# Kernel tuning notes

Measured on AMD Instinct MI355X. Metric: run time of the kernel, lower is better.

The kernel has to match this reference:

```python
import jax, jax.numpy as jnp
import numpy as np

B, NP, K = 8, 512, 64   # graphs, points per graph, knn neighbors
N = B * NP              # total nodes
EPS = 1e-5


def knn_edges(pos):
    """knn_graph(pos, k=K, batch, loop=True): edges (src=j neighbor, dst=i)."""
    p = pos.reshape(B, NP, 3)
    d2 = jnp.sum((p[:, :, None, :] - p[:, None, :, :]) ** 2, axis=-1)  # [B,NP,NP]
    _, idx = jax.lax.top_k(-d2, K)  # [B,NP,K] nearest (self included, d2=0)
    off = (jnp.arange(B, dtype=jnp.int32) * NP)[:, None, None]
    src = (idx.astype(jnp.int32) + off).reshape(-1)
    dst = jnp.broadcast_to(jnp.arange(NP, dtype=jnp.int32)[None, :, None] + off,
                           (B, NP, K)).reshape(-1)
    return src, dst


def graph_norm(x, batch, w, b, ms):
    """PyG GraphNorm: per-graph mean/std with learnable mean scale."""
    cnt = jax.ops.segment_sum(jnp.ones((x.shape[0], 1), x.dtype), batch, B)
    mean = jax.ops.segment_sum(x, batch, B) / cnt
    out = x - mean[batch] * ms
    var = jax.ops.segment_sum(out * out, batch, B) / cnt
    return w * out / jnp.sqrt(var + EPS)[batch] + b


def pointnet_layer(h, pos, src, dst, w1, b1, w2, b2):
    """message = MLP(concat(h_j, pos_j - pos_i)); aggregate = scatter-max over dst."""
    m = jnp.concatenate([h[src], pos[src] - pos[dst]], axis=-1)  # [E, Cin+3]
    m = jax.nn.relu(m @ w1 + b1) @ w2 + b2                        # [E, Cout]
    return jax.ops.segment_max(m, dst, N)


def _forward(batch, pos,
             gn1_w, gn1_b, gn1_ms, gn2_w, gn2_b, gn2_ms, gn3_w, gn3_b, gn3_ms,
             gn4_w, gn4_b, gn4_ms, gn5_w, gn5_b, gn5_ms, gn6_w, gn6_b, gn6_ms,
             c1_w1, c1_b1, c1_w2, c1_b2, c2_w1, c2_b1, c2_w2, c2_b2,
             c3_w1, c3_b1, c3_w2, c3_b2, c4_w1, c4_b1, c4_w2, c4_b2,
             c5_w1, c5_b1, c5_w2, c5_b2, cls_w, cls_b):
    src, dst = knn_edges(pos)
    h = graph_norm(pos, batch, gn1_w, gn1_b, gn1_ms)
    h = pointnet_layer(h, pos, src, dst, c1_w1, c1_b1, c1_w2, c1_b2)
    h = jax.nn.relu(graph_norm(h, batch, gn2_w, gn2_b, gn2_ms))
    h = pointnet_layer(h, pos, src, dst, c2_w1, c2_b1, c2_w2, c2_b2)
    h = jax.nn.relu(graph_norm(h, batch, gn3_w, gn3_b, gn3_ms))
    h = pointnet_layer(h, pos, src, dst, c3_w1, c3_b1, c3_w2, c3_b2)
    h = jax.nn.relu(graph_norm(h, batch, gn4_w, gn4_b, gn4_ms))
    h = pointnet_layer(h, pos, src, dst, c4_w1, c4_b1, c4_w2, c4_b2)
    h = jax.nn.relu(graph_norm(h, batch, gn5_w, gn5_b, gn5_ms))
    h = pointnet_layer(h, pos, src, dst, c5_w1, c5_b1, c5_w2, c5_b2)
    h = jax.nn.relu(graph_norm(h, batch, gn6_w, gn6_b, gn6_ms))
    return h @ cls_w + cls_b  # [N, 14]


def setup_inputs() -> dict:
    key = jax.random.key(0)
    ks = iter(jax.random.split(key, 40))
    inp = {}
    inp["pos"] = jax.random.normal(next(ks), (N, 3), jnp.float32)
    inp["batch"] = jnp.repeat(jnp.arange(B, dtype=jnp.int32), NP)
    for i, c in enumerate([3, 64, 128, 256, 512, 512], 1):
        inp[f"gn{i}_w"] = jnp.ones((c,), jnp.float32)
        inp[f"gn{i}_b"] = jnp.zeros((c,), jnp.float32)
        inp[f"gn{i}_ms"] = jnp.ones((c,), jnp.float32)
    for i, (ci, co) in enumerate([(3, 64), (64, 128), (128, 256), (256, 512), (512, 512)], 1):
        fin = ci + 3
        inp[f"c{i}_w1"] = jax.random.normal(next(ks), (fin, co), jnp.float32) / np.sqrt(fin).astype(np.float32)
        inp[f"c{i}_b1"] = jnp.zeros((co,), jnp.float32)
        inp[f"c{i}_w2"] = jax.random.normal(next(ks), (co, co), jnp.float32) / np.sqrt(co).astype(np.float32)
        inp[f"c{i}_b2"] = jnp.zeros((co,), jnp.float32)
    inp["cls_w"] = jax.random.normal(next(ks), (512, 14), jnp.float32) / np.float32(np.sqrt(512))
    inp["cls_b"] = jnp.zeros((14,), jnp.float32)
    return inp


def reference(pos, batch,
              gn1_w, gn1_b, gn1_ms, gn2_w, gn2_b, gn2_ms, gn3_w, gn3_b, gn3_ms,
              gn4_w, gn4_b, gn4_ms, gn5_w, gn5_b, gn5_ms, gn6_w, gn6_b, gn6_ms,
              c1_w1, c1_b1, c1_w2, c1_b2, c2_w1, c2_b1, c2_w2, c2_b2,
              c3_w1, c3_b1, c3_w2, c3_b2, c4_w1, c4_b1, c4_w2, c4_b2,
              c5_w1, c5_b1, c5_w2, c5_b2, cls_w, cls_b):
    return _forward(batch, pos,
                    gn1_w, gn1_b, gn1_ms, gn2_w, gn2_b, gn2_ms, gn3_w, gn3_b, gn3_ms,
                    gn4_w, gn4_b, gn4_ms, gn5_w, gn5_b, gn5_ms, gn6_w, gn6_b, gn6_ms,
                    c1_w1, c1_b1, c1_w2, c1_b2, c2_w1, c2_b1, c2_w2, c2_b2,
                    c3_w1, c3_b1, c3_w2, c3_b2, c4_w1, c4_b1, c4_w2, c4_b2,
                    c5_w1, c5_b1, c5_w2, c5_b2, cls_w, cls_b)
```

## Files before the change

### kernel.cpp

```cpp
#include <hip/hip_runtime.h>
#include <stdint.h>

#define N_NODES 4096
#define NGRAPH 8
#define NPTS 512
#define KNN 64
#define EPSN 1e-5f

typedef _Float16 f16x8 __attribute__((ext_vector_type(8)));
typedef float f32x4 __attribute__((ext_vector_type(4)));
typedef unsigned long long u64;

__device__ __forceinline__ unsigned short f2h(float f) {
    _Float16 h = (_Float16)f;
    union { _Float16 h; unsigned short u; } cv; cv.h = h;
    return cv.u;
}

__device__ __forceinline__ void w2cv(const float* __restrict__ src, unsigned short* __restrict__ dst,
                                     int off, int lg2c) {
    int C = 1 << lg2c;
    int k = off >> lg2c, n = off & (C - 1);
    int d = ((n >> 4) * (C / 32) + (k >> 5)) * 512 + ((k >> 3) & 3) * 128 + (n & 15) * 8 + (k & 7);
    dst[d] = f2h(src[off]);
}

__global__ __launch_bounds__(64) void setup_kernel(const float* __restrict__ pos, int* __restrict__ knn_out,
                                                   const float* __restrict__ wa, const float* __restrict__ wb,
                                                   const float* __restrict__ wc, const float* __restrict__ wd,
                                                   const float* __restrict__ we,
                                                   unsigned short* __restrict__ oa, unsigned short* __restrict__ ob,
                                                   unsigned short* __restrict__ oc, unsigned short* __restrict__ od,
                                                   unsigned short* __restrict__ oe,
                                                   float* __restrict__ statz,
                                                   const float* __restrict__ ms1, const float* __restrict__ gw1,
                                                   float* __restrict__ Aa, float* __restrict__ Sa) {
#pragma clang fp contract(off)
    __shared__ float px[NPTS], py[NPTS], pz[NPTS];
    __shared__ u64 keys[NPTS];
    int bid = blockIdx.x;
    int tid = threadIdx.x;
    int gidx = bid * 64 + tid;
    for (int idx = gidx; idx < 40960; idx += 262144) statz[idx] = 0.f;
    for (int idx = gidx; idx < 610304; idx += 262144) {
        if (idx < 4096)        w2cv(wa, oa, idx, 6);
        else if (idx < 20480)  w2cv(wb, ob, idx - 4096, 7);
        else if (idx < 86016)  w2cv(wc, oc, idx - 20480, 8);
        else if (idx < 348160) w2cv(wd, od, idx - 86016, 9);
        else                   w2cv(we, oe, idx - 348160, 9);
    }
    if (bid < 24) {
        int g = bid / 3, ch = bid - g * 3;
        float s1 = 0.f, s2 = 0.f;
        for (int n = tid; n < NPTS; n += 64) {
            float v = pos[(g * NPTS + n) * 3 + ch];
            s1 += v; s2 += v * v;
        }
        #pragma unroll
        for (int off = 32; off; off >>= 1) { s1 += __shfl_xor(s1, off); s2 += __shfl_xor(s2, off); }
        if (tid == 0) {
            float mean = s1 * (1.f / NPTS);
            float av = mean * ms1[ch];
            float var = s2 * (1.f / NPTS) - 2.f * av * mean + av * av;
            Aa[g * 3 + ch] = av;
            Sa[g * 3 + ch] = gw1[ch] / sqrtf(var + EPSN);
        }
    }
    int b = bid >> 9;
    int il = bid & (NPTS - 1);
    for (int n = tid; n < NPTS; n += 64) {
        int base = (b * NPTS + n) * 3;
        px[n] = pos[base]; py[n] = pos[base + 1]; pz[n] = pos[base + 2];
    }
    __syncthreads();
    float xi = px[il], yi = py[il], zi = pz[il];
    for (int n = tid; n < NPTS; n += 64) {
        float dx = px[n] - xi, dy = py[n] - yi, dz = pz[n] - zi;
        float d2 = dx * dx;
        d2 = d2 + dy * dy;
        d2 = d2 + dz * dz;
        keys[n] = (((u64)__float_as_uint(d2)) << 32) | (unsigned)n;
    }
    __syncthreads();
    for (int k2 = 2; k2 <= NPTS; k2 <<= 1) {
        for (int j = k2 >> 1; j > 0; j >>= 1) {
            #pragma unroll 4
            for (int p = 0; p < 4; ++p) {
                int pid = tid + p * 64;
                int t = ((pid & ~(j - 1)) << 1) | (pid & (j - 1));
                int ixj = t | j;
                u64 a = keys[t], c = keys[ixj];
                bool up = ((t & k2) == 0);
                if ((a > c) == up) { keys[t] = c; keys[ixj] = a; }
            }
            __syncthreads();
        }
    }
    int j0 = (int)(keys[tid] & 0xffffffffu);
    knn_out[(size_t)(b * NPTS + il) * KNN + tid] = b * NPTS + j0;
}

template<int CIN, int C, int RELU, int RAW>
__global__ __launch_bounds__(C) void node_kernel(const float* __restrict__ y, const float* __restrict__ pos,
                                                 const float* __restrict__ p1, const float* __restrict__ p2,
                                                 const float* __restrict__ ms, const float* __restrict__ gw,
                                                 const float* __restrict__ bnp,
                                                 const float* __restrict__ w1, const float* __restrict__ b1,
                                                 float* __restrict__ U, float* __restrict__ P) {
    constexpr int ROWS = 16;
    constexpr int KC = 64;
    constexpr int LDH = KC + 4;
    __shared__ float hs[ROWS][LDH];
    __shared__ float As_[CIN > 0 ? CIN : 1], Ss_[CIN > 0 ? CIN : 1];
    const int c = threadIdx.x;
    const int n0 = blockIdx.x * ROWS;
    const int b = n0 >> 9;
    if (RAW) {
        for (int ch = c; ch < CIN; ch += C) {
            float s1 = p1[b * CIN + ch], s2 = p2[b * CIN + ch];
            float mean = s1 * (1.f / NPTS);
            float a = mean * ms[ch];
            float var = s2 * (1.f / NPTS) - 2.f * a * mean + a * a;
            As_[ch] = a;
            Ss_[ch] = gw[ch] / sqrtf(var + EPSN);
        }
    }
    float acc[ROWS];
    #pragma unroll
    for (int r = 0; r < ROWS; ++r) acc[r] = 0.f;
    constexpr int NCHUNK = (CIN + KC - 1) / KC;
    #pragma unroll 1
    for (int s = 0; s < NCHUNK; ++s) {
        const int k0 = s * KC;
        const int kc = (CIN - k0 < KC) ? (CIN - k0) : KC;
        __syncthreads();
        for (int idx = c; idx < ROWS * kc; idx += C) {
            int r = idx / kc, k = idx - r * kc;
            int ch = k0 + k;
            float a = RAW ? As_[ch] : p1[b * CIN + ch];
            float sf = RAW ? Ss_[ch] : p2[b * CIN + ch];
            float v = (y[(size_t)(n0 + r) * CIN + ch] - a) * sf + bnp[ch];
            if (RELU) v = fmaxf(v, 0.f);
            hs[r][k] = v;
        }
        __syncthreads();
        int k = 0;
        for (; k + 4 <= kc; k += 4) {
            float w0 = w1[(size_t)(k0 + k) * C + c];
            float w1v = w1[(size_t)(k0 + k + 1) * C + c];
            float w2v = w1[(size_t)(k0 + k + 2) * C + c];
            float w3v = w1[(size_t)(k0 + k + 3) * C + c];
            #pragma unroll
            for (int r = 0; r < ROWS; ++r) {
                f32x4 hv = *(const f32x4*)&hs[r][k];
                acc[r] = fmaf(hv[0], w0, acc[r]);
                acc[r] = fmaf(hv[1], w1v, acc[r]);
                acc[r] = fmaf(hv[2], w2v, acc[r]);
                acc[r] = fmaf(hv[3], w3v, acc[r]);
            }
        }
        for (; k < kc; ++k) {
            float wv = w1[(size_t)(k0 + k) * C + c];
            #pragma unroll
            for (int r = 0; r < ROWS; ++r)
                acc[r] = fmaf(hs[r][k], wv, acc[r]);
        }
    }
    float pacc[ROWS];
    #pragma unroll
    for (int r = 0; r < ROWS; ++r) pacc[r] = 0.f;
    #pragma unroll
    for (int e = 0; e < 3; ++e) {
        float wv = w1[(size_t)(CIN + e) * C + c];
        #pragma unroll
        for (int r = 0; r < ROWS; ++r)
            pacc[r] = fmaf(pos[(n0 + r) * 3 + e], wv, pacc[r]);
    }
    float bv = b1[c];
    #pragma unroll
    for (int r = 0; r < ROWS; ++r) {
        U[(size_t)(n0 + r) * C + c] = acc[r] + pacc[r] + bv;
        P[(size_t)(n0 + r) * C + c] = pacc[r];
    }
}

template<int C, int W>
__global__ __launch_bounds__(W * 64, 4) void edge_kernel(const float* __restrict__ U, const float* __restrict__ P,
                                                         const int* __restrict__ knn, const unsigned short* __restrict__ w2t,
                                                         const float* __restrict__ b2, float* __restrict__ Y,
                                                         float* __restrict__ sum1, float* __restrict__ sum2) {
    constexpr int NCT = C / (W * 16);
    constexpr int S32 = C / 32;
    constexpr int NCHUNK = C / 8;
    __shared__ unsigned short Th[64 * C];
    __shared__ int jn[64];
    __shared__ float Pr[C];
    const int bid = blockIdx.x;
    const int i = ((bid & 7) << 9) | (bid >> 3);
    const int tid = threadIdx.x;
    const int wave = tid >> 6, lane = tid & 63, m = lane & 15, quad = lane >> 4;
    const int cw = wave * (NCT * 16);
    if (tid < 64) jn[tid] = knn[(size_t)i * KNN + tid];
    for (int idx = tid; idx < C; idx += W * 64) Pr[idx] = P[(size_t)i * C + idx];
    __syncthreads();
    #pragma unroll 2
    for (int idx = tid; idx < 64 * NCHUNK; idx += W * 64) {
        int row = idx / NCHUNK, ch = idx - row * NCHUNK;
        const float* up = U + (size_t)jn[row] * C + ch * 8;
        f32x4 va = *(const f32x4*)up;
        f32x4 vb = *(const f32x4*)(up + 4);
        f32x4 pa = *(const f32x4*)&Pr[ch * 8];
        f32x4 pb = *(const f32x4*)&Pr[ch * 8 + 4];
        uint4 pk;
        pk.x = (unsigned)f2h(fmaxf(va[0] - pa[0], 0.f)) | ((unsigned)f2h(fmaxf(va[1] - pa[1], 0.f)) << 16);
        pk.y = (unsigned)f2h(fmaxf(va[2] - pa[2], 0.f)) | ((unsigned)f2h(fmaxf(va[3] - pa[3], 0.f)) << 16);
        pk.z = (unsigned)f2h(fmaxf(vb[0] - pb[0], 0.f)) | ((unsigned)f2h(fmaxf(vb[1] - pb[1], 0.f)) << 16);
        pk.w = (unsigned)f2h(fmaxf(vb[2] - pb[2], 0.f)) | ((unsigned)f2h(fmaxf(vb[3] - pb[3], 0.f)) << 16);
        int sc = (ch & ~7) | ((ch ^ row) & 7);
        *(uint4*)&Th[row * C + sc * 8] = pk;
    }
    __syncthreads();
    f32x4 acc[4][NCT];
    f32x4 zero = {0.f, 0.f, 0.f, 0.f};
    #pragma unroll
    for (int rt = 0; rt < 4; ++rt)
        #pragma unroll
        for (int ct = 0; ct < NCT; ++ct)
            acc[rt][ct] = zero;
    #pragma unroll 2
    for (int s = 0; s < S32; ++s) {
        f16x8 a[4];
        #pragma unroll
        for (int rt = 0; rt < 4; ++rt) {
            int row = rt * 16 + m;
            int chunk = s * 4 + quad;
            int sc = (chunk & ~7) | ((chunk ^ row) & 7);
            a[rt] = *(const f16x8*)&Th[row * C + sc * 8];
        }
        #pragma unroll
        for (int ct = 0; ct < NCT; ++ct) {
            const f16x8 bb = *(const f16x8*)(w2t +
                (size_t)(((cw >> 4) + ct) * S32 + s) * 512 + quad * 128 + m * 8);
            #pragma unroll
            for (int rt = 0; rt < 4; ++rt)
                acc[rt][ct] = __builtin_amdgcn_mfma_f32_16x16x32_f16(a[rt], bb, acc[rt][ct], 0, 0, 0);
        }
    }
    const int gb = i >> 9;
    #pragma unroll
    for (int ct = 0; ct < NCT; ++ct) {
        float vmax = -3.4e38f;
        #pragma unroll
        for (int rt = 0; rt < 4; ++rt) {
            vmax = fmaxf(vmax, acc[rt][ct][0]);
            vmax = fmaxf(vmax, acc[rt][ct][1]);
            vmax = fmaxf(vmax, acc[rt][ct][2]);
            vmax = fmaxf(vmax, acc[rt][ct][3]);
        }
        vmax = fmaxf(vmax, __shfl_xor(vmax, 16));
        vmax = fmaxf(vmax, __shfl_xor(vmax, 32));
        if (quad == 0) {
            int col = cw + ct * 16 + m;
            float val = vmax + b2[col];
            Y[(size_t)i * C + col] = val;
            atomicAdd(&sum1[gb * C + col], val);
            atomicAdd(&sum2[gb * C + col], val * val);
        }
    }
}

__device__ __forceinline__ uint4 pack8(f32x4 va, f32x4 vb, f32x4 pa, f32x4 pb) {
    uint4 pk;
    pk.x = (unsigned)f2h(fmaxf(va[0] - pa[0], 0.f)) | ((unsigned)f2h(fmaxf(va[1] - pa[1], 0.f)) << 16);
    pk.y = (unsigned)f2h(fmaxf(va[2] - pa[2], 0.f)) | ((unsigned)f2h(fmaxf(va[3] - pa[3], 0.f)) << 16);
    pk.z = (unsigned)f2h(fmaxf(vb[0] - pb[0], 0.f)) | ((unsigned)f2h(fmaxf(vb[1] - pb[1], 0.f)) << 16);
    pk.w = (unsigned)f2h(fmaxf(vb[2] - pb[2], 0.f)) | ((unsigned)f2h(fmaxf(vb[3] - pb[3], 0.f)) << 16);
    return pk;
}

template<int C>
__global__ __launch_bounds__(512, 2) void edgeb_kernel(const float* __restrict__ U, const float* __restrict__ P,
                                                       const int* __restrict__ knn, const unsigned short* __restrict__ w2t,
                                                       const float* __restrict__ b2, float* __restrict__ Y,
                                                       float* __restrict__ sum1, float* __restrict__ sum2) {
    constexpr int NCT = C / 128;
    constexpr int S32 = C / 32;
    constexpr int NCHK = C / 8;
    constexpr int RSTEP = 512 / NCHK;
    __shared__ unsigned short Th[(C / 64) * 128 * 64];
    __shared__ int jn[128];
    const int bid = blockIdx.x;
    const int g = bid & 7;
    const int n0 = (g << 9) | ((bid >> 3) << 1);
    const int tid = threadIdx.x;
    const int lane = tid & 63, wave = tid >> 6, m = lane & 15, quad = lane >> 4;
    const int cw = wave * (NCT * 16);
    if (tid < 128) jn[tid] = knn[(size_t)(n0 + (tid >> 6)) * KNN + (tid & 63)];
    const int ch = tid & (NCHK - 1);
    const int rb = tid / NCHK;
    const int cblk = ch >> 3, cw8 = ch & 7;
    const float* pp = P + (size_t)n0 * C + ch * 8;
    f32x4 pa0 = *(const f32x4*)pp;
    f32x4 pb0 = *(const f32x4*)(pp + 4);
    f32x4 pa1 = *(const f32x4*)(pp + C);
    f32x4 pb1 = *(const f32x4*)(pp + C + 4);
    __syncthreads();
    #pragma unroll 4
    for (int t = 0; t < 128 / RSTEP; ++t) {
        int row = rb + t * RSTEP;
        const float* up = U + (size_t)jn[row] * C + ch * 8;
        f32x4 va = *(const f32x4*)up;
        f32x4 vb = *(const f32x4*)(up + 4);
        f32x4 pa = (row & 64) ? pa1 : pa0;
        f32x4 pb = (row & 64) ? pb1 : pb0;
        *(uint4*)&Th[cblk * 8192 + row * 64 + ((cw8 ^ (row & 7)) << 3)] = pack8(va, vb, pa, pb);
    }
    __syncthreads();
    f32x4 acc[8][NCT];
    f32x4 zero = {0.f, 0.f, 0.f, 0.f};
    #pragma unroll
    for (int rt = 0; rt < 8; ++rt)
        #pragma unroll
        for (int ct = 0; ct < NCT; ++ct)
            acc[rt][ct] = zero;
    const unsigned short* wt = w2t + (size_t)(cw >> 4) * S32 * 512 + quad * 128 + m * 8;
    int idx0[8], idx1[8];
    #pragma unroll
    for (int rt = 0; rt < 8; ++rt) {
        int row = rt * 16 + m;
        idx0[rt] = row * 64 + ((quad ^ (row & 7)) << 3);
        idx1[rt] = row * 64 + (((4 + quad) ^ (row & 7)) << 3);
    }
    const unsigned short* pB[NCT];
    #pragma unroll
    for (int ct = 0; ct < NCT; ++ct)
        pB[ct] = wt + ((size_t)ct * S32 + 2) * 512;
    f16x8 bbA[NCT], bbB[NCT];
    #pragma unroll
    for (int ct = 0; ct < NCT; ++ct) {
        bbA[ct] = *(const f16x8*)(wt + (size_t)ct * S32 * 512);
        bbB[ct] = *(const f16x8*)(wt + ((size_t)ct * S32 + 1) * 512);
    }
    const unsigned short* tcur = Th;
    auto step = [&](f16x8 (&buf)[NCT], const int (&idx)[8], int poff, bool pre) {
        f16x8 a[8];
        #pragma unroll
        for (int rt = 0; rt < 8; ++rt)
            a[rt] = *(const f16x8*)&tcur[idx[rt]];
        #pragma unroll
        for (int ct = 0; ct < NCT; ++ct) {
            f16x8 bcur = buf[ct];
            if (pre) buf[ct] = *(const f16x8*)(pB[ct] + poff);
            __builtin_amdgcn_s_setprio(1);
            #pragma unroll
            for (int rt = 0; rt < 8; ++rt)
                acc[rt][ct] = __builtin_amdgcn_mfma_f32_16x16x32_f16(a[rt], bcur, acc[rt][ct], 0, 0, 0);
            __builtin_amdgcn_s_setprio(0);
        }
    };
    #pragma unroll 1
    for (int s = 0; s + 2 < S32; s += 2) {
        step(bbA, idx0, 0, true);
        step(bbB, idx1, 512, true);
        tcur += 8192;
        #pragma unroll
        for (int ct = 0; ct < NCT; ++ct) pB[ct] += 1024;
    }
    step(bbA, idx0, 0, false);
    step(bbB, idx1, 0, false);
    #pragma unroll
    for (int h = 0; h < 2; ++h) {
        #pragma unroll
        for (int ct = 0; ct < NCT; ++ct) {
            float vmax = -3.4e38f;
            #pragma unroll
            for (int rt = h * 4; rt < h * 4 + 4; ++rt) {
                vmax = fmaxf(vmax, acc[rt][ct][0]);
                vmax = fmaxf(vmax, acc[rt][ct][1]);
                vmax = fmaxf(vmax, acc[rt][ct][2]);
                vmax = fmaxf(vmax, acc[rt][ct][3]);
            }
            vmax = fmaxf(vmax, __shfl_xor(vmax, 16));
            vmax = fmaxf(vmax, __shfl_xor(vmax, 32));
            if (quad == 0) {
                int col = cw + ct * 16 + m;
                float val = vmax + b2[col];
                Y[(size_t)(n0 + h) * C + col] = val;
                atomicAdd(&sum1[g * C + col], val);
                atomicAdd(&sum2[g * C + col], val * val);
            }
        }
    }
}

__global__ __launch_bounds__(256) void cls_kernel(const float* __restrict__ y, const float* __restrict__ sum1,
                                                  const float* __restrict__ sum2, const float* __restrict__ ms,
                                                  const float* __restrict__ gw, const float* __restrict__ gnb,
                                                  const float* __restrict__ w, const float* __restrict__ bias,
                                                  float* __restrict__ out) {
    __shared__ float wl[512 * 14];
    __shared__ _Float16 hn[16][520];
    __shared__ float As[512], Ss[512];
    int tid = threadIdx.x;
    int n0 = blockIdx.x * 16;
    int b = n0 >> 9;
    for (int ch = tid; ch < 512; ch += 256) {
        float s1 = sum1[b * 512 + ch], s2 = sum2[b * 512 + ch];
        float mean = s1 * (1.f / NPTS);
        float a = mean * ms[ch];
        float var = s2 * (1.f / NPTS) - 2.f * a * mean + a * a;
        As[ch] = a;
        Ss[ch] = gw[ch] / sqrtf(var + EPSN);
    }
    for (int idx = tid; idx < 512 * 14; idx += 256) wl[idx] = w[idx];
    __syncthreads();
    for (int idx = tid; idx < 16 * 512; idx += 256) {
        int r = idx >> 9, k = idx & 511;
        float v = (y[(size_t)(n0 + r) * 512 + k] - As[k]) * Ss[k] + gnb[k];
        hn[r][k] = (_Float16)fmaxf(v, 0.f);
    }
    __syncthreads();
    if (tid < 224) {
        int nl = tid / 14, c = tid - nl * 14;
        float acc = bias[c];
        for (int k = 0; k < 512; ++k)
            acc += (float)hn[nl][k] * wl[k * 14 + c];
        out[(size_t)(n0 + nl) * 14 + c] = acc;
    }
}

extern "C" void kernel_launch(void* const* d_in, const int* in_sizes, int n_in,
                              void* d_out, int out_size, void* d_ws, size_t ws_size,
                              hipStream_t stream) {
    const float* pos = (const float*)d_in[0];
    const float* gnw[6]; const float* gnb[6]; const float* gnms[6];
    for (int i = 0; i < 6; ++i) {
        gnw[i]  = (const float*)d_in[2 + 3 * i];
        gnb[i]  = (const float*)d_in[3 + 3 * i];
        gnms[i] = (const float*)d_in[4 + 3 * i];
    }
    const float* cw1[5]; const float* cb1[5]; const float* cw2[5]; const float* cb2[5];
    for (int i = 0; i < 5; ++i) {
        cw1[i] = (const float*)d_in[20 + 4 * i];
        cb1[i] = (const float*)d_in[21 + 4 * i];
        cw2[i] = (const float*)d_in[22 + 4 * i];
        cb2[i] = (const float*)d_in[23 + 4 * i];
    }
    const float* clsw = (const float*)d_in[40];
    const float* clsb = (const float*)d_in[41];
    float* out = (float*)d_out;

    char* ws = (char*)d_ws;
    int* knn             = (int*)(ws + 0);
    float* U             = (float*)(ws + 1048576);
    float* P             = (float*)(ws + 9437184);
    float* y             = (float*)(ws + 26214400);
    float* Aa            = (float*)(ws + 34603008);
    float* Sa            = (float*)(ws + 34619392);
    unsigned short* w2t0 = (unsigned short*)(ws + 34635776);
    unsigned short* w2t1 = (unsigned short*)(ws + 34643968);
    unsigned short* w2t2 = (unsigned short*)(ws + 34676736);
    unsigned short* w2t3 = (unsigned short*)(ws + 34807808);
    unsigned short* w2t4 = (unsigned short*)(ws + 35332096);
    float* acc           = (float*)(ws + 35856384);
    float* s1l[5]; float* s2l[5];
    for (int l = 0; l < 5; ++l) { s1l[l] = acc + l * 8192; s2l[l] = s1l[l] + 4096; }

    setup_kernel<<<N_NODES, 64, 0, stream>>>(pos, knn, cw2[0], cw2[1], cw2[2], cw2[3], cw2[4],
                                             w2t0, w2t1, w2t2, w2t3, w2t4, acc,
                                             gnms[0], gnw[0], Aa, Sa);

    node_kernel<3, 64, 0, 0><<<N_NODES / 16, 64, 0, stream>>>(pos, pos, Aa, Sa, gnms[0], gnw[0], gnb[0], cw1[0], cb1[0], U, P);
    edge_kernel<64, 4><<<N_NODES, 256, 0, stream>>>(U, P, knn, w2t0, cb2[0], y, s1l[0], s2l[0]);

    node_kernel<64, 128, 1, 1><<<N_NODES / 16, 128, 0, stream>>>(y, pos, s1l[0], s2l[0], gnms[1], gnw[1], gnb[1], cw1[1], cb1[1], U, P);
    edge_kernel<128, 8><<<N_NODES, 512, 0, stream>>>(U, P, knn, w2t1, cb2[1], y, s1l[1], s2l[1]);

    node_kernel<128, 256, 1, 1><<<N_NODES / 16, 256, 0, stream>>>(y, pos, s1l[1], s2l[1], gnms[2], gnw[2], gnb[2], cw1[2], cb1[2], U, P);
    edgeb_kernel<256><<<N_NODES / 2, 512, 0, stream>>>(U, P, knn, w2t2, cb2[2], y, s1l[2], s2l[2]);

    node_kernel<256, 512, 1, 1><<<N_NODES / 16, 512, 0, stream>>>(y, pos, s1l[2], s2l[2], gnms[3], gnw[3], gnb[3], cw1[3], cb1[3], U, P);
    edgeb_kernel<512><<<N_NODES / 2, 512, 0, stream>>>(U, P, knn, w2t3, cb2[3], y, s1l[3], s2l[3]);

    node_kernel<512, 512, 1, 1><<<N_NODES / 16, 512, 0, stream>>>(y, pos, s1l[3], s2l[3], gnms[4], gnw[4], gnb[4], cw1[4], cb1[4], U, P);
    edgeb_kernel<512><<<N_NODES / 2, 512, 0, stream>>>(U, P, knn, w2t4, cb2[4], y, s1l[4], s2l[4]);

    cls_kernel<<<N_NODES / 16, 256, 0, stream>>>(y, s1l[4], s2l[4], gnms[5], gnw[5], gnb[5], clsw, clsb, out);
}
```

Baseline: 698.2 us.

## Split edgeb rows across two wave groups with 1024-thread blocks

The edgeb kernel now launches 1024 threads, or 16 waves, per block. Each group of 8 waves handles one of the two destination nodes' 64 neighbor rows, so each wave keeps 4 row tiles of accumulators instead of 8. This halves accumulator register pressure per wave and doubles the waves available for latency hiding. In exchange, each B-matrix fragment is loaded by twice as many waves, and the launch bound of 1024 threads with 4 blocks per SM may force register spilling.

```diff
diff --git a/kernel.cpp b/kernel.cpp
--- a/kernel.cpp
+++ b/kernel.cpp
@@ -279,14 +279,14 @@
 }
 
 template<int C>
-__global__ __launch_bounds__(512, 2) void edgeb_kernel(const float* __restrict__ U, const float* __restrict__ P,
-                                                       const int* __restrict__ knn, const unsigned short* __restrict__ w2t,
-                                                       const float* __restrict__ b2, float* __restrict__ Y,
-                                                       float* __restrict__ sum1, float* __restrict__ sum2) {
+__global__ __launch_bounds__(1024, 4) void edgeb_kernel(const float* __restrict__ U, const float* __restrict__ P,
+                                                        const int* __restrict__ knn, const unsigned short* __restrict__ w2t,
+                                                        const float* __restrict__ b2, float* __restrict__ Y,
+                                                        float* __restrict__ sum1, float* __restrict__ sum2) {
     constexpr int NCT = C / 128;
     constexpr int S32 = C / 32;
     constexpr int NCHK = C / 8;
-    constexpr int RSTEP = 512 / NCHK;
+    constexpr int RSTEP = 1024 / NCHK;
     __shared__ unsigned short Th[(C / 64) * 128 * 64];
     __shared__ int jn[128];
     const int bid = blockIdx.x;
@@ -294,7 +294,9 @@
     const int n0 = (g << 9) | ((bid >> 3) << 1);
     const int tid = threadIdx.x;
     const int lane = tid & 63, wave = tid >> 6, m = lane & 15, quad = lane >> 4;
-    const int cw = wave * (NCT * 16);
+    const int wrow = wave >> 3;
+    const int wcol = wave & 7;
+    const int cw = wcol * (NCT * 16);
     if (tid < 128) jn[tid] = knn[(size_t)(n0 + (tid >> 6)) * KNN + (tid & 63)];
     const int ch = tid & (NCHK - 1);
     const int rb = tid / NCHK;
@@ -316,79 +318,71 @@
         *(uint4*)&Th[cblk * 8192 + row * 64 + ((cw8 ^ (row & 7)) << 3)] = pack8(va, vb, pa, pb);
     }
     __syncthreads();
-    f32x4 acc[8][NCT];
+    f32x4 acc[4][NCT];
     f32x4 zero = {0.f, 0.f, 0.f, 0.f};
     #pragma unroll
-    for (int rt = 0; rt < 8; ++rt)
+    for (int rt = 0; rt < 4; ++rt)
         #pragma unroll
         for (int ct = 0; ct < NCT; ++ct)
             acc[rt][ct] = zero;
     const unsigned short* wt = w2t + (size_t)(cw >> 4) * S32 * 512 + quad * 128 + m * 8;
-    int idx0[8], idx1[8];
-    #pragma unroll
-    for (int rt = 0; rt < 8; ++rt) {
-        int row = rt * 16 + m;
+    int idx0[4];
+    #pragma unroll
+    for (int rt = 0; rt < 4; ++rt) {
+        int row = wrow * 64 + rt * 16 + m;
         idx0[rt] = row * 64 + ((quad ^ (row & 7)) << 3);
-        idx1[rt] = row * 64 + (((4 + quad) ^ (row & 7)) << 3);
     }
     const unsigned short* pB[NCT];
     #pragma unroll
     for (int ct = 0; ct < NCT; ++ct)
-        pB[ct] = wt + ((size_t)ct * S32 + 2) * 512;
-    f16x8 bbA[NCT], bbB[NCT];
-    #pragma unroll
-    for (int ct = 0; ct < NCT; ++ct) {
-        bbA[ct] = *(const f16x8*)(wt + (size_t)ct * S32 * 512);
-        bbB[ct] = *(const f16x8*)(wt + ((size_t)ct * S32 + 1) * 512);
-    }
+        pB[ct] = wt + ((size_t)ct * S32 + 1) * 512;
+    f16x8 bb[NCT];
+    #pragma unroll
+    for (int ct = 0; ct < NCT; ++ct)
+        bb[ct] = *(const f16x8*)(wt + (size_t)ct * S32 * 512);
     const unsigned short* tcur = Th;
-    auto step = [&](f16x8 (&buf)[NCT], const int (&idx)[8], int poff, bool pre) {
-        f16x8 a[8];
-        #pragma unroll
-        for (int rt = 0; rt < 8; ++rt)
-            a[rt] = *(const f16x8*)&tcur[idx[rt]];
+    auto stepf = [&](int axor, int poff, bool pre) {
+        f16x8 a[4];
+        #pragma unroll
+        for (int rt = 0; rt < 4; ++rt)
+            a[rt] = *(const f16x8*)&tcur[idx0[rt] ^ axor];
         #pragma unroll
         for (int ct = 0; ct < NCT; ++ct) {
-            f16x8 bcur = buf[ct];
-            if (pre) buf[ct] = *(const f16x8*)(pB[ct] + poff);
+            f16x8 bcur = bb[ct];
+            if (pre) bb[ct] = *(const f16x8*)(pB[ct] + poff);
             __builtin_amdgcn_s_setprio(1);
             #pragma unroll
-            for (int rt = 0; rt < 8; ++rt)
+            for (int rt = 0; rt < 4; ++rt)
                 acc[rt][ct] = __builtin_amdgcn_mfma_f32_16x16x32_f16(a[rt], bcur, acc[rt][ct], 0, 0, 0);
             __builtin_amdgcn_s_setprio(0);
         }
     };
     #pragma unroll 1
-    for (int s = 0; s + 2 < S32; s += 2) {
-        step(bbA, idx0, 0, true);
-        step(bbB, idx1, 512, true);
+    for (int s = 0; s + 2 <= S32; s += 2) {
+        stepf(0, 0, true);
+        stepf(32, 512, s + 2 < S32);
         tcur += 8192;
         #pragma unroll
         for (int ct = 0; ct < NCT; ++ct) pB[ct] += 1024;
     }
-    step(bbA, idx0, 0, false);
-    step(bbB, idx1, 0, false);
-    #pragma unroll
-    for (int h = 0; h < 2; ++h) {
-        #pragma unroll
-        for (int ct = 0; ct < NCT; ++ct) {
-            float vmax = -3.4e38f;
-            #pragma unroll
-            for (int rt = h * 4; rt < h * 4 + 4; ++rt) {
-                vmax = fmaxf(vmax, acc[rt][ct][0]);
-                vmax = fmaxf(vmax, acc[rt][ct][1]);
-                vmax = fmaxf(vmax, acc[rt][ct][2]);
-                vmax = fmaxf(vmax, acc[rt][ct][3]);
-            }
-            vmax = fmaxf(vmax, __shfl_xor(vmax, 16));
-            vmax = fmaxf(vmax, __shfl_xor(vmax, 32));
-            if (quad == 0) {
-                int col = cw + ct * 16 + m;
-                float val = vmax + b2[col];
-                Y[(size_t)(n0 + h) * C + col] = val;
-                atomicAdd(&sum1[g * C + col], val);
-                atomicAdd(&sum2[g * C + col], val * val);
-            }
+    #pragma unroll
+    for (int ct = 0; ct < NCT; ++ct) {
+        float vmax = -3.4e38f;
+        #pragma unroll
+        for (int rt = 0; rt < 4; ++rt) {
+            vmax = fmaxf(vmax, acc[rt][ct][0]);
+            vmax = fmaxf(vmax, acc[rt][ct][1]);
+            vmax = fmaxf(vmax, acc[rt][ct][2]);
+            vmax = fmaxf(vmax, acc[rt][ct][3]);
+        }
+        vmax = fmaxf(vmax, __shfl_xor(vmax, 16));
+        vmax = fmaxf(vmax, __shfl_xor(vmax, 32));
+        if (quad == 0) {
+            int col = cw + ct * 16 + m;
+            float val = vmax + b2[col];
+            Y[(size_t)(n0 + wrow) * C + col] = val;
+            atomicAdd(&sum1[g * C + col], val);
+            atomicAdd(&sum2[g * C + col], val * val);
         }
     }
 }
@@ -477,13 +471,13 @@
     edge_kernel<128, 8><<<N_NODES, 512, 0, stream>>>(U, P, knn, w2t1, cb2[1], y, s1l[1], s2l[1]);
 
     node_kernel<128, 256, 1, 1><<<N_NODES / 16, 256, 0, stream>>>(y, pos, s1l[1], s2l[1], gnms[2], gnw[2], gnb[2], cw1[2], cb1[2], U, P);
-    edgeb_kernel<256><<<N_NODES / 2, 512, 0, stream>>>(U, P, knn, w2t2, cb2[2], y, s1l[2], s2l[2]);
+    edgeb_kernel<256><<<N_NODES / 2, 1024, 0, stream>>>(U, P, knn, w2t2, cb2[2], y, s1l[2], s2l[2]);
 
     node_kernel<256, 512, 1, 1><<<N_NODES / 16, 512, 0, stream>>>(y, pos, s1l[2], s2l[2], gnms[3], gnw[3], gnb[3], cw1[3], cb1[3], U, P);
-    edgeb_kernel<512><<<N_NODES / 2, 512, 0, stream>>>(U, P, knn, w2t3, cb2[3], y, s1l[3], s2l[3]);
+    edgeb_kernel<512><<<N_NODES / 2, 1024, 0, stream>>>(U, P, knn, w2t3, cb2[3], y, s1l[3], s2l[3]);
 
     node_kernel<512, 512, 1, 1><<<N_NODES / 16, 512, 0, stream>>>(y, pos, s1l[3], s2l[3], gnms[4], gnw[4], gnb[4], cw1[4], cb1[4], U, P);
-    edgeb_kernel<512><<<N_NODES / 2, 512, 0, stream>>>(U, P, knn, w2t4, cb2[4], y, s1l[4], s2l[4]);
+    edgeb_kernel<512><<<N_NODES / 2, 1024, 0, stream>>>(U, P, knn, w2t4, cb2[4], y, s1l[4], s2l[4]);
 
     cls_kernel<<<N_NODES / 16, 256, 0, stream>>>(y, s1l[4], s2l[4], gnms[5], gnw[5], gnb[5], clsw, clsb, out);
 }
```

After: 732.1 us. +4.9%, slower.
